# Kernel optimization log

Measured on AMD Instinct MI355X. Metric: run time of the kernel, lower is better.

## Reference

```python
import jax, jax.numpy as jnp
import numpy as np

K2 = 4.0 / 3.0; K4 = 4.10451; K5 = 19.08857; K6 = 254.5553148552
KN = 7.5; WF = 6.0; GA = 3.0; GC = 2.0
BOHR = 0.5291772105638411; HARTREE = 27.211386024367243
C2BOHR = 1.0 / BOHR; C2EV = 0.5 * HARTREE
N_ATOMS = 50000; N_NEIGH = 48; ZMAX = 87; NREF = 7; NFREQ = 23; KCN = 7


def _sp_inv(x):
    # softplus_inverse
    return jnp.float32(np.log(np.expm1(x)))


def setup_inputs() -> dict:
    key = jax.random.key(0)
    ks = jax.random.split(key, 24)
    P = N_ATOMS * N_NEIGH
    u = lambda k, shp, lo, hi: jax.random.uniform(k, shp, jnp.float32, lo, hi)
    Z = jax.random.randint(ks[0], (N_ATOMS,), 0, ZMAX)
    idx_i = jnp.repeat(jnp.arange(N_ATOMS), N_NEIGH)  # center index per pair
    idx_j = jax.random.randint(ks[1], (P,), 0, N_ATOMS)
    r_ij = u(ks[2], (P,), 1.5, 6.0)  # Angstrom
    qa = 0.05 * jax.random.normal(ks[3], (N_ATOMS,), jnp.float32)
    return dict(
        Z=Z, idx_i=idx_i, idx_j=idx_j, r_ij=r_ij, qa=qa,
        s6_raw=_sp_inv(1.0), s8_raw=_sp_inv(1.61679827),
        a1_raw=_sp_inv(0.44959224), a2_raw=_sp_inv(3.35743605),
        scaleq_raw=_sp_inv(1.0),
        refsys=jax.random.randint(ks[4], (ZMAX, NREF), 0, ZMAX),
        zeff=u(ks[5], (ZMAX,), 1.0, 10.0),
        refh=u(ks[6], (ZMAX, NREF), 0.0, 0.3),
        sscale=u(ks[7], (ZMAX,), 0.5, 1.5),
        secaiw=u(ks[8], (ZMAX, NFREQ), 0.0, 1.0),
        gam=u(ks[9], (ZMAX,), 0.05, 0.5),
        ascale=u(ks[10], (ZMAX, NREF), 0.5, 1.5),
        alphaiw=u(ks[11], (ZMAX, NREF, NFREQ), 0.0, 5.0),
        hcount=u(ks[12], (ZMAX, NREF), 0.0, 2.0),
        casimir_polder_weights=u(ks[13], (NFREQ,), 0.0, 0.5),
        rcov=u(ks[14], (ZMAX,), 0.6, 2.5),
        en=u(ks[15], (ZMAX,), 0.5, 4.0),
        ncount_mask=(u(ks[16], (ZMAX, NREF, KCN), 0.0, 1.0) < 0.6).astype(jnp.float32),
        ncount_weight=u(ks[17], (ZMAX, NREF, KCN), 0.5, 2.0),
        cn=u(ks[18], (ZMAX, NREF, KCN), 0.0, 6.0),
        fixgweights=(lambda g: g / jnp.sum(g, -1, keepdims=True))(u(ks[19], (ZMAX, NREF), 0.1, 1.0)),
        refq=u(ks[20], (ZMAX, NREF), -0.2, 0.2),
        sqrt_r4r2=u(ks[21], (ZMAX,), 1.0, 4.0),
    )


def compute_refc6(scaleq, refsys, zeff, refh, sscale, secaiw, gam, ascale, alphaiw, hcount, cpw):
    iz = zeff[refsys]                                   # [Z, nref]
    qref = iz
    qmod = iz + refh * scaleq
    qmod_ = jnp.where(qmod > 1e-8, qmod, 1.0)
    zeta = jnp.where(qmod > 1e-8,
                     jnp.exp(GA * (1.0 - jnp.exp(gam[refsys] * GC * (1.0 - qref / qmod_)))),
                     np.exp(GA).astype(np.float32))
    asec = sscale[refsys][..., None] * secaiw[refsys] * zeta[..., None]  # [Z,nref,nfreq]
    alpha = jnp.maximum(ascale[..., None] * (alphaiw - hcount[..., None] * asec), 0.0)
    return (3.0 / np.pi) * jnp.einsum('iax,jbx,x->ijab', alpha, alpha, cpw)  # [Z,Z,nref,nref]


def reference(Z, idx_i, idx_j, r_ij, qa, s6_raw, s8_raw, a1_raw, a2_raw, scaleq_raw,
              refsys, zeff, refh, sscale, secaiw, gam, ascale, alphaiw, hcount,
              casimir_polder_weights, rcov, en, ncount_mask, ncount_weight, cn,
              fixgweights, refq, sqrt_r4r2):
    n_atoms = qa.shape[0]
    scaleq = jax.nn.softplus(scaleq_raw)
    # refc6 is computed under no_grad in the original module
    refc6 = jax.lax.stop_gradient(compute_refc6(scaleq, refsys, zeff, refh, sscale,
                                                secaiw, gam, ascale, alphaiw, hcount,
                                                casimir_polder_weights))
    r = r_ij * C2BOHR
    Zi = Z[idx_i]; Zj = Z[idx_j]
    # coordination-number contribution per pair, scattered to centers
    rco = K2 * (rcov[Zi] + rcov[Zj])
    den = K4 * jnp.exp(-(jnp.abs(en[Zi] - en[Zj]) + K5) ** 2 / K6)
    tmp = den * 0.5 * (1.0 + jax.lax.erf(-KN * (r - rco) / rco))
    covcn = jax.ops.segment_sum(tmp, idx_i, num_segments=n_atoms)
    # gaussian reference-CN weights [n_atoms, nref]
    gweights = jnp.sum(ncount_mask[Z] * jnp.exp(-WF * ncount_weight[Z] * (covcn[:, None, None] - cn[Z]) ** 2), -1)
    norm = jnp.sum(gweights, -1, keepdims=True)
    gweights = jnp.where(norm > 1e-8, gweights / jnp.where(norm > 1e-8, norm, 1.0), fixgweights[Z])
    # charge scaling zeta [n_atoms, nref]
    iz = zeff[Z][:, None]
    qref = iz + refq[Z] * scaleq
    qmod = iz + qa[:, None]
    qmod_ = jnp.where(qmod > 1e-8, qmod, 1.0)
    zeta = jnp.where(qmod > 1e-8,
                     jnp.exp(GA * (1.0 - jnp.exp(gam[Z][:, None] * GC * (1.0 - qref / qmod_)))),
                     np.exp(GA).astype(np.float32)) * gweights
    zetai = zeta[idx_i]; zetaj = zeta[idx_j]            # [P, nref]
    refc6ij = refc6[Zi, Zj]                             # [P, nref, nref]
    c6ij = jnp.einsum('pab,pa,pb->p', refc6ij, zetai, zetaj)
    r4r2ij = np.float32(np.sqrt(3.0)) * sqrt_r4r2[Zi] * sqrt_r4r2[Zj]
    a1 = jax.nn.softplus(a1_raw); a2 = jax.nn.softplus(a2_raw)
    r0 = a1 * r4r2ij + a2
    oor6 = 1.0 / (r ** 6 + r0 ** 6)
    oor8 = 1.0 / (r ** 8 + r0 ** 8)
    s6 = jax.nn.softplus(s6_raw); s8 = jax.nn.softplus(s8_raw)
    edisp = -c6ij * (s6 * oor6 + s8 * r4r2ij ** 2 * oor8) * C2EV
    eatom = jax.ops.segment_sum(edisp, idx_i, num_segments=n_atoms)
    zeros = jnp.zeros((n_atoms,), r_ij.dtype)  # compute_atomic_quantities=False
    return (eatom, zeros, zeros)
```

## Files before the change

kernel.cpp:

```cpp
#include <hip/hip_runtime.h>
#include <hip/hip_fp16.h>
#include <math.h>

#define NATOMS 50000
#define NNEIGH 48
#define ZMAXV 87
#define NREFV 7
#define NFREQV 23
#define KCNV 7
#define XPAD 24
#define XPADH 32
#define ATOMS_PER_BLOCK 4
#define PAIR_BLOCK (ATOMS_PER_BLOCK * NNEIGH)

#define C2BOHR 1.8897261258369282f
#define C2EV 13.605693012183622f
#define K2C 1.33333333333333333f
#define K4C 4.10451f
#define K5C 19.08857f
#define K6INV (1.0f / 254.5553148552f)
#define KNC 7.5f
#define EXP_GA 20.085536923187668f
#define QRT3 1.3160740129524924f

__device__ __forceinline__ float sp(float x) { return log1pf(expf(x)); }

__global__ __launch_bounds__(256) void k_setup(
    const int* __restrict__ Z, const int* __restrict__ refsys,
    const float* __restrict__ zeff, const float* __restrict__ refh,
    const float* __restrict__ sscale, const float* __restrict__ secaiw,
    const float* __restrict__ gam, const float* __restrict__ ascale,
    const float* __restrict__ alphaiw, const float* __restrict__ hcount,
    const float* __restrict__ rcov, const float* __restrict__ en,
    const float* __restrict__ s6r, const float* __restrict__ s8r,
    const float* __restrict__ a1r, const float* __restrict__ a2r,
    const float* __restrict__ sqr,
    float* __restrict__ scal_out, float* __restrict__ alpha_out,
    float2* __restrict__ re2_out, float* __restrict__ zero_out)
{
    int e = blockIdx.x * 256 + threadIdx.x;
    if (e == 0) {
        scal_out[0] = sp(s6r[0]);
        scal_out[1] = sp(s8r[0]);
        scal_out[2] = sp(a1r[0]);
        scal_out[3] = sp(a2r[0]);
    }
    if (e < 2 * NATOMS) zero_out[e] = 0.0f;
    if (e < NATOMS) {
        int z = Z[e];
        re2_out[e] = make_float2(rcov[z], en[z]);
    }
    if (e < ZMAXV * NREFV * XPAD) {
        int x = e % XPAD;
        int za = e / XPAD;
        float v = 0.0f;
        if (x < NFREQV) {
            float scaleq = sp(sqr[0]);
            int rs = refsys[za];
            float iz = zeff[rs];
            float qmod = iz + refh[za] * scaleq;
            float zeta = (qmod > 1e-8f)
                ? __expf(3.0f * (1.0f - __expf(gam[rs] * 2.0f * (1.0f - iz / qmod))))
                : EXP_GA;
            float asec = sscale[rs] * secaiw[rs * NFREQV + x] * zeta;
            v = fmaxf(ascale[za] * (alphaiw[za * NFREQV + x] - hcount[za] * asec), 0.0f);
        }
        alpha_out[e] = v;
    }
}

__global__ __launch_bounds__(PAIR_BLOCK) void k_atoms(
    const int* __restrict__ Z, const int* __restrict__ idx_j,
    const float* __restrict__ r_ij, const float* __restrict__ qa,
    const float* __restrict__ sqr, const float* __restrict__ zeff,
    const float* __restrict__ gam, const float2* __restrict__ re2,
    const float* __restrict__ nmask, const float* __restrict__ nweight,
    const float* __restrict__ cn, const float* __restrict__ fixg,
    const float* __restrict__ refq, const float* __restrict__ cpw,
    const float* __restrict__ alpha_tab, const float* __restrict__ sr4r2,
    __half* __restrict__ A_out)
{
    __shared__ float sh[PAIR_BLOCK];
    __shared__ float covcn[ATOMS_PER_BLOCK];
    __shared__ float gwl[ATOMS_PER_BLOCK][NREFV];
    __shared__ float ztl[ATOMS_PER_BLOCK][NREFV];
    const int t = threadIdx.x;
    const int a0 = blockIdx.x * ATOMS_PER_BLOCK;

    {
        int p = blockIdx.x * PAIR_BLOCK + t;
        int atom = a0 + (t / NNEIGH);
        float2 rei = re2[atom];
        float2 rej = re2[idx_j[p]];
        float r = r_ij[p] * C2BOHR;
        float rco = K2C * (rei.x + rej.x);
        float d = fabsf(rei.y - rej.y) + K5C;
        float den = K4C * __expf(-d * d * K6INV);
        sh[t] = den * 0.5f * (1.0f + erff(-KNC * (r - rco) / rco));
    }
    __syncthreads();
    if (t < ATOMS_PER_BLOCK) {
        float s = 0.0f;
        for (int k = 0; k < NNEIGH; k++) s += sh[t * NNEIGH + k];
        covcn[t] = s;
    }
    __syncthreads();

    if (t < ATOMS_PER_BLOCK * NREFV) {
        int al = t / NREFV, a = t % NREFV;
        int zl = Z[a0 + al];
        float cc = covcn[al];
        const float* mB = nmask + (zl * NREFV + a) * KCNV;
        const float* wB = nweight + (zl * NREFV + a) * KCNV;
        const float* cB = cn + (zl * NREFV + a) * KCNV;
        float g = 0.0f;
        for (int k = 0; k < KCNV; k++) {
            float dc = cc - cB[k];
            g += mB[k] * __expf(-6.0f * wB[k] * dc * dc);
        }
        gwl[al][a] = g;
    }
    __syncthreads();

    if (t < ATOMS_PER_BLOCK * NREFV) {
        int al = t / NREFV, a = t % NREFV;
        int zl = Z[a0 + al];
        float norm = 0.0f;
        for (int b = 0; b < NREFV; b++) norm += gwl[al][b];
        float w = (norm > 1e-8f) ? (gwl[al][a] / norm) : fixg[zl * NREFV + a];
        float scaleq = sp(sqr[0]);
        float iz = zeff[zl];
        float qref = iz + refq[zl * NREFV + a] * scaleq;
        float qmod = iz + qa[a0 + al];
        float zeta = (qmod > 1e-8f)
            ? __expf(3.0f * (1.0f - __expf(gam[zl] * 2.0f * (1.0f - qref / qmod))))
            : EXP_GA;
        ztl[al][a] = zeta * w;
    }
    __syncthreads();

    if (t < ATOMS_PER_BLOCK * XPADH) {
        int al = t / XPADH, x = t % XPADH;
        int zl = Z[a0 + al];
        float v = 0.0f;
        if (x < NFREQV) {
            float s = 0.0f;
            #pragma unroll
            for (int a = 0; a < NREFV; a++)
                s += ztl[al][a] * alpha_tab[(zl * NREFV + a) * XPAD + x];
            v = s * sqrtf(cpw[x] * 0.9549296585513721f);
        } else if (x == NFREQV) {
            v = QRT3 * sr4r2[zl];
        }
        A_out[(size_t)a0 * XPADH + t] = __float2half(v);
    }
}

__global__ __launch_bounds__(PAIR_BLOCK) void k_pairs(
    const int* __restrict__ idx_j, const float* __restrict__ r_ij,
    const float* __restrict__ scal, const __half* __restrict__ Ah,
    float* __restrict__ eatom)
{
    __shared__ float sh[PAIR_BLOCK];
    __shared__ float Ai[ATOMS_PER_BLOCK][NFREQV];
    __shared__ float Asi[ATOMS_PER_BLOCK];
    const int t = threadIdx.x;
    const int a0 = blockIdx.x * ATOMS_PER_BLOCK;

    if (t < ATOMS_PER_BLOCK * XPADH) {
        int al = t >> 5, x = t & 31;
        float v = __half2float(Ah[(size_t)a0 * XPADH + t]);
        if (x < NFREQV) Ai[al][x] = v;
        else if (x == NFREQV) Asi[al] = v;
    }
    __syncthreads();

    const float s6 = scal[0], s8 = scal[1], a1 = scal[2], a2 = scal[3];

    int p = blockIdx.x * PAIR_BLOCK + t;
    int al = t / NNEIGH;
    int j = idx_j[p];
    float r = r_ij[p] * C2BOHR;

    const float4* Aj4 = (const float4*)(Ah + (size_t)j * XPADH);
    float4 w0 = Aj4[0], w1 = Aj4[1], w2 = Aj4[2];
    float a[24];
    {
        const __half2* h0 = (const __half2*)&w0;
        const __half2* h1 = (const __half2*)&w1;
        const __half2* h2 = (const __half2*)&w2;
        #pragma unroll
        for (int k = 0; k < 4; k++) {
            float2 f0 = __half22float2(h0[k]);
            float2 f1 = __half22float2(h1[k]);
            float2 f2 = __half22float2(h2[k]);
            a[2 * k]      = f0.x; a[2 * k + 1]      = f0.y;
            a[8 + 2 * k]  = f1.x; a[8 + 2 * k + 1]  = f1.y;
            a[16 + 2 * k] = f2.x; a[16 + 2 * k + 1] = f2.y;
        }
    }
    float c6 = 0.0f;
    #pragma unroll
    for (int x = 0; x < NFREQV; x++) c6 += a[x] * Ai[al][x];
    float sj = a[NFREQV];

    float r4r2 = Asi[al] * sj;
    float r0 = a1 * r4r2 + a2;
    float r2 = r * r, r4 = r2 * r2, r6 = r4 * r2, r8 = r4 * r4;
    float p2 = r0 * r0, p4 = p2 * p2, p6 = p4 * p2, p8 = p4 * p4;
    float oor6 = 1.0f / (r6 + p6);
    float oor8 = 1.0f / (r8 + p8);
    float e = -c6 * (s6 * oor6 + s8 * r4r2 * r4r2 * oor8) * C2EV;

    sh[t] = e;
    __syncthreads();
    if (t < ATOMS_PER_BLOCK) {
        float s = 0.0f;
        for (int k = 0; k < NNEIGH; k++) s += sh[t * NNEIGH + k];
        eatom[a0 + t] = s;
    }
}

extern "C" void kernel_launch(void* const* d_in, const int* in_sizes, int n_in,
                              void* d_out, int out_size, void* d_ws, size_t ws_size,
                              hipStream_t stream)
{
    const int*   Z       = (const int*)  d_in[0];
    const int*   idx_j   = (const int*)  d_in[2];
    const float* r_ij    = (const float*)d_in[3];
    const float* qa      = (const float*)d_in[4];
    const float* s6r     = (const float*)d_in[5];
    const float* s8r     = (const float*)d_in[6];
    const float* a1r     = (const float*)d_in[7];
    const float* a2r     = (const float*)d_in[8];
    const float* sqraw   = (const float*)d_in[9];
    const int*   refsys  = (const int*)  d_in[10];
    const float* zeff    = (const float*)d_in[11];
    const float* refh    = (const float*)d_in[12];
    const float* sscale  = (const float*)d_in[13];
    const float* secaiw  = (const float*)d_in[14];
    const float* gam     = (const float*)d_in[15];
    const float* ascale  = (const float*)d_in[16];
    const float* alphaiw = (const float*)d_in[17];
    const float* hcount  = (const float*)d_in[18];
    const float* cpw     = (const float*)d_in[19];
    const float* rcov    = (const float*)d_in[20];
    const float* en      = (const float*)d_in[21];
    const float* nmask   = (const float*)d_in[22];
    const float* nweight = (const float*)d_in[23];
    const float* cn      = (const float*)d_in[24];
    const float* fixg    = (const float*)d_in[25];
    const float* refq    = (const float*)d_in[26];
    const float* sr4r2   = (const float*)d_in[27];

    float* ws    = (float*)d_ws;
    float* scal  = ws;
    float* alpha = ws + 16;
    float2* re2  = (float2*)(ws + 16 + ZMAXV * NREFV * XPAD);
    __half* Ah   = (__half*)(ws + 16 + ZMAXV * NREFV * XPAD + 2 * NATOMS);

    float* eatom = (float*)d_out;
    float* zeros = eatom + NATOMS;

    k_setup<<<391, 256, 0, stream>>>(Z, refsys, zeff, refh, sscale, secaiw, gam,
                                     ascale, alphaiw, hcount, rcov, en,
                                     s6r, s8r, a1r, a2r, sqraw,
                                     scal, alpha, re2, zeros);
    k_atoms<<<NATOMS / ATOMS_PER_BLOCK, PAIR_BLOCK, 0, stream>>>(
        Z, idx_j, r_ij, qa, sqraw, zeff, gam, re2,
        nmask, nweight, cn, fixg, refq, cpw, alpha, sr4r2, Ah);
    k_pairs<<<NATOMS / ATOMS_PER_BLOCK, PAIR_BLOCK, 0, stream>>>(
        idx_j, r_ij, scal, Ah, eatom);
}
```

Before: 177.7 us.

## Process two pairs per thread with eight atoms per block in atom and pair kernels

Each block now covers 8 atoms with 192 threads, and every thread handles two neighbor pairs (p and p+192) in both the coordination-number pass and the C6/energy pass. The atom-descriptor writes switch to half2 stores, and the workspace offsets are realigned with hard-coded byte offsets. The aim is more memory-level parallelism per thread, since each thread has two independent gathers in flight, and fewer blocks. In exchange there is more register pressure and fewer threads overall, and the fixed offsets rely on the workspace layout matching.

After: 180.1 us. Within noise of the previous version (+1.3%).

```diff
diff --git a/kernel.cpp b/kernel.cpp
--- a/kernel.cpp
+++ b/kernel.cpp
@@ -10,8 +10,9 @@
 #define KCNV 7
 #define XPAD 24
 #define XPADH 32
-#define ATOMS_PER_BLOCK 4
-#define PAIR_BLOCK (ATOMS_PER_BLOCK * NNEIGH)
+#define APB 8
+#define TPB 192
+#define PPB (APB * NNEIGH)
 
 #define C2BOHR 1.8897261258369282f
 #define C2EV 13.605693012183622f
@@ -69,7 +70,7 @@
     }
 }
 
-__global__ __launch_bounds__(PAIR_BLOCK) void k_atoms(
+__global__ __launch_bounds__(TPB) void k_atoms(
     const int* __restrict__ Z, const int* __restrict__ idx_j,
     const float* __restrict__ r_ij, const float* __restrict__ qa,
     const float* __restrict__ sqr, const float* __restrict__ zeff,
@@ -78,35 +79,49 @@
     const float* __restrict__ cn, const float* __restrict__ fixg,
     const float* __restrict__ refq, const float* __restrict__ cpw,
     const float* __restrict__ alpha_tab, const float* __restrict__ sr4r2,
-    __half* __restrict__ A_out)
+    __half2* __restrict__ A_out2)
 {
-    __shared__ float sh[PAIR_BLOCK];
-    __shared__ float covcn[ATOMS_PER_BLOCK];
-    __shared__ float gwl[ATOMS_PER_BLOCK][NREFV];
-    __shared__ float ztl[ATOMS_PER_BLOCK][NREFV];
+    __shared__ float sh[PPB];
+    __shared__ float covcn[APB];
+    __shared__ float gwl[APB][NREFV];
+    __shared__ float ztl[APB][NREFV];
     const int t = threadIdx.x;
-    const int a0 = blockIdx.x * ATOMS_PER_BLOCK;
-
-    {
-        int p = blockIdx.x * PAIR_BLOCK + t;
-        int atom = a0 + (t / NNEIGH);
-        float2 rei = re2[atom];
-        float2 rej = re2[idx_j[p]];
-        float r = r_ij[p] * C2BOHR;
-        float rco = K2C * (rei.x + rej.x);
-        float d = fabsf(rei.y - rej.y) + K5C;
-        float den = K4C * __expf(-d * d * K6INV);
-        sh[t] = den * 0.5f * (1.0f + erff(-KNC * (r - rco) / rco));
-    }
-    __syncthreads();
-    if (t < ATOMS_PER_BLOCK) {
+    const int a0 = blockIdx.x * APB;
+
+    {
+        int p0 = blockIdx.x * PPB + t;
+        int p1 = p0 + TPB;
+        int al0 = t / NNEIGH;
+        int j0 = idx_j[p0];
+        int j1 = idx_j[p1];
+        float rr0 = r_ij[p0];
+        float rr1 = r_ij[p1];
+        float2 rej0 = re2[j0];
+        float2 rej1 = re2[j1];
+        float2 rei0 = re2[a0 + al0];
+        float2 rei1 = re2[a0 + al0 + 4];
+
+        float r0 = rr0 * C2BOHR;
+        float rco0 = K2C * (rei0.x + rej0.x);
+        float d0 = fabsf(rei0.y - rej0.y) + K5C;
+        float den0 = K4C * __expf(-d0 * d0 * K6INV);
+        sh[t] = den0 * 0.5f * (1.0f + erff(-KNC * (r0 - rco0) / rco0));
+
+        float r1 = rr1 * C2BOHR;
+        float rco1 = K2C * (rei1.x + rej1.x);
+        float d1 = fabsf(rei1.y - rej1.y) + K5C;
+        float den1 = K4C * __expf(-d1 * d1 * K6INV);
+        sh[t + TPB] = den1 * 0.5f * (1.0f + erff(-KNC * (r1 - rco1) / rco1));
+    }
+    __syncthreads();
+    if (t < APB) {
         float s = 0.0f;
         for (int k = 0; k < NNEIGH; k++) s += sh[t * NNEIGH + k];
         covcn[t] = s;
     }
     __syncthreads();
 
-    if (t < ATOMS_PER_BLOCK * NREFV) {
+    if (t < APB * NREFV) {
         int al = t / NREFV, a = t % NREFV;
         int zl = Z[a0 + al];
         float cc = covcn[al];
@@ -122,7 +137,7 @@
     }
     __syncthreads();
 
-    if (t < ATOMS_PER_BLOCK * NREFV) {
+    if (t < APB * NREFV) {
         int al = t / NREFV, a = t % NREFV;
         int zl = Z[a0 + al];
         float norm = 0.0f;
@@ -139,82 +154,112 @@
     }
     __syncthreads();
 
-    if (t < ATOMS_PER_BLOCK * XPADH) {
-        int al = t / XPADH, x = t % XPADH;
+    if (t < APB * (XPADH / 2)) {
+        int al = t >> 4, xh = t & 15;
+        int x0 = 2 * xh, x1 = 2 * xh + 1;
         int zl = Z[a0 + al];
-        float v = 0.0f;
-        if (x < NFREQV) {
+        float v0 = 0.0f, v1 = 0.0f;
+        if (x0 < NFREQV) {
             float s = 0.0f;
             #pragma unroll
             for (int a = 0; a < NREFV; a++)
-                s += ztl[al][a] * alpha_tab[(zl * NREFV + a) * XPAD + x];
-            v = s * sqrtf(cpw[x] * 0.9549296585513721f);
-        } else if (x == NFREQV) {
-            v = QRT3 * sr4r2[zl];
-        }
-        A_out[(size_t)a0 * XPADH + t] = __float2half(v);
+                s += ztl[al][a] * alpha_tab[(zl * NREFV + a) * XPAD + x0];
+            v0 = s * sqrtf(cpw[x0] * 0.9549296585513721f);
+        }
+        if (x1 < NFREQV) {
+            float s = 0.0f;
+            #pragma unroll
+            for (int a = 0; a < NREFV; a++)
+                s += ztl[al][a] * alpha_tab[(zl * NREFV + a) * XPAD + x1];
+            v1 = s * sqrtf(cpw[x1] * 0.9549296585513721f);
+        } else if (x1 == NFREQV) {
+            v1 = QRT3 * sr4r2[zl];
+        }
+        A_out2[(size_t)(a0 + al) * (XPADH / 2) + xh] = __floats2half2_rn(v0, v1);
     }
 }
 
-__global__ __launch_bounds__(PAIR_BLOCK) void k_pairs(
+__global__ __launch_bounds__(TPB) void k_pairs(
     const int* __restrict__ idx_j, const float* __restrict__ r_ij,
     const float* __restrict__ scal, const __half* __restrict__ Ah,
     float* __restrict__ eatom)
 {
-    __shared__ float sh[PAIR_BLOCK];
-    __shared__ float Ai[ATOMS_PER_BLOCK][NFREQV];
-    __shared__ float Asi[ATOMS_PER_BLOCK];
+    __shared__ float sh[PPB];
+    __shared__ float Ai[APB][NFREQV];
+    __shared__ float Asi[APB];
     const int t = threadIdx.x;
-    const int a0 = blockIdx.x * ATOMS_PER_BLOCK;
-
-    if (t < ATOMS_PER_BLOCK * XPADH) {
-        int al = t >> 5, x = t & 31;
-        float v = __half2float(Ah[(size_t)a0 * XPADH + t]);
+    const int a0 = blockIdx.x * APB;
+
+    {
+        int al = t / XPAD, x = t - al * XPAD;
+        float v = __half2float(Ah[(size_t)(a0 + al) * XPADH + x]);
         if (x < NFREQV) Ai[al][x] = v;
-        else if (x == NFREQV) Asi[al] = v;
+        else Asi[al] = v;
     }
     __syncthreads();
 
     const float s6 = scal[0], s8 = scal[1], a1 = scal[2], a2 = scal[3];
 
-    int p = blockIdx.x * PAIR_BLOCK + t;
-    int al = t / NNEIGH;
-    int j = idx_j[p];
-    float r = r_ij[p] * C2BOHR;
-
-    const float4* Aj4 = (const float4*)(Ah + (size_t)j * XPADH);
-    float4 w0 = Aj4[0], w1 = Aj4[1], w2 = Aj4[2];
-    float a[24];
-    {
-        const __half2* h0 = (const __half2*)&w0;
-        const __half2* h1 = (const __half2*)&w1;
-        const __half2* h2 = (const __half2*)&w2;
+    int p0 = blockIdx.x * PPB + t;
+    int p1 = p0 + TPB;
+    int al0 = t / NNEIGH;
+    int al1 = al0 + 4;
+    int j0 = idx_j[p0];
+    int j1 = idx_j[p1];
+    float rr0 = r_ij[p0];
+    float rr1 = r_ij[p1];
+
+    const float4* P0 = (const float4*)(Ah + (size_t)j0 * XPADH);
+    const float4* P1 = (const float4*)(Ah + (size_t)j1 * XPADH);
+    float4 u0 = P0[0], u1 = P0[1], u2 = P0[2];
+    float4 w0 = P1[0], w1 = P1[1], w2 = P1[2];
+
+    float c60 = 0.0f, c61 = 0.0f, sj0, sj1;
+    {
+        const __half2* hu = (const __half2*)&u0;
+        const __half2* a2p[3] = { (const __half2*)&u0, (const __half2*)&u1, (const __half2*)&u2 };
+        const __half2* b2p[3] = { (const __half2*)&w0, (const __half2*)&w1, (const __half2*)&w2 };
+        (void)hu;
         #pragma unroll
-        for (int k = 0; k < 4; k++) {
-            float2 f0 = __half22float2(h0[k]);
-            float2 f1 = __half22float2(h1[k]);
-            float2 f2 = __half22float2(h2[k]);
-            a[2 * k]      = f0.x; a[2 * k + 1]      = f0.y;
-            a[8 + 2 * k]  = f1.x; a[8 + 2 * k + 1]  = f1.y;
-            a[16 + 2 * k] = f2.x; a[16 + 2 * k + 1] = f2.y;
-        }
-    }
-    float c6 = 0.0f;
-    #pragma unroll
-    for (int x = 0; x < NFREQV; x++) c6 += a[x] * Ai[al][x];
-    float sj = a[NFREQV];
-
-    float r4r2 = Asi[al] * sj;
-    float r0 = a1 * r4r2 + a2;
-    float r2 = r * r, r4 = r2 * r2, r6 = r4 * r2, r8 = r4 * r4;
-    float p2 = r0 * r0, p4 = p2 * p2, p6 = p4 * p2, p8 = p4 * p4;
-    float oor6 = 1.0f / (r6 + p6);
-    float oor8 = 1.0f / (r8 + p8);
-    float e = -c6 * (s6 * oor6 + s8 * r4r2 * r4r2 * oor8) * C2EV;
-
-    sh[t] = e;
-    __syncthreads();
-    if (t < ATOMS_PER_BLOCK) {
+        for (int seg = 0; seg < 3; seg++) {
+            #pragma unroll
+            for (int k = 0; k < 4; k++) {
+                int x = seg * 8 + 2 * k;
+                float2 fa = __half22float2(a2p[seg][k]);
+                float2 fb = __half22float2(b2p[seg][k]);
+                if (x < NFREQV)      c60 += fa.x * Ai[al0][x];
+                else                 sj0 = fa.x;
+                if (x + 1 < NFREQV)  c60 += fa.y * Ai[al0][x + 1];
+                else if (x + 1 == NFREQV) sj0 = fa.y;
+                if (x < NFREQV)      c61 += fb.x * Ai[al1][x];
+                if (x + 1 < NFREQV)  c61 += fb.y * Ai[al1][x + 1];
+                else if (x + 1 == NFREQV) sj1 = fb.y;
+            }
+        }
+    }
+
+    float e0, e1;
+    {
+        float r = rr0 * C2BOHR;
+        float r4r2 = Asi[al0] * sj0;
+        float r0v = a1 * r4r2 + a2;
+        float r2 = r * r, r4 = r2 * r2, r6 = r4 * r2, r8 = r4 * r4;
+        float p2 = r0v * r0v, p4 = p2 * p2, p6 = p4 * p2, p8 = p4 * p4;
+        e0 = -c60 * (s6 / (r6 + p6) + s8 * r4r2 * r4r2 / (r8 + p8)) * C2EV;
+    }
+    {
+        float r = rr1 * C2BOHR;
+        float r4r2 = Asi[al1] * sj1;
+        float r0v = a1 * r4r2 + a2;
+        float r2 = r * r, r4 = r2 * r2, r6 = r4 * r2, r8 = r4 * r4;
+        float p2 = r0v * r0v, p4 = p2 * p2, p6 = p4 * p2, p8 = p4 * p4;
+        e1 = -c61 * (s6 / (r6 + p6) + s8 * r4r2 * r4r2 / (r8 + p8)) * C2EV;
+    }
+
+    sh[t] = e0;
+    sh[t + TPB] = e1;
+    __syncthreads();
+    if (t < APB) {
         float s = 0.0f;
         for (int k = 0; k < NNEIGH; k++) s += sh[t * NNEIGH + k];
         eatom[a0 + t] = s;
@@ -253,11 +298,11 @@
     const float* refq    = (const float*)d_in[26];
     const float* sr4r2   = (const float*)d_in[27];
 
-    float* ws    = (float*)d_ws;
-    float* scal  = ws;
-    float* alpha = ws + 16;
-    float2* re2  = (float2*)(ws + 16 + ZMAXV * NREFV * XPAD);
-    __half* Ah   = (__half*)(ws + 16 + ZMAXV * NREFV * XPAD + 2 * NATOMS);
+    char* wsb = (char*)d_ws;
+    float*  scal  = (float*)(wsb);
+    float*  alpha = (float*)(wsb + 64);
+    float2* re2   = (float2*)(wsb + 58528);
+    __half* Ah    = (__half*)(wsb + 458752);
 
     float* eatom = (float*)d_out;
     float* zeros = eatom + NATOMS;
@@ -266,9 +311,9 @@
                                      ascale, alphaiw, hcount, rcov, en,
                                      s6r, s8r, a1r, a2r, sqraw,
                                      scal, alpha, re2, zeros);
-    k_atoms<<<NATOMS / ATOMS_PER_BLOCK, PAIR_BLOCK, 0, stream>>>(
+    k_atoms<<<NATOMS / APB, TPB, 0, stream>>>(
         Z, idx_j, r_ij, qa, sqraw, zeff, gam, re2,
-        nmask, nweight, cn, fixg, refq, cpw, alpha, sr4r2, Ah);
-    k_pairs<<<NATOMS / ATOMS_PER_BLOCK, PAIR_BLOCK, 0, stream>>>(
+        nmask, nweight, cn, fixg, refq, cpw, alpha, sr4r2, (__half2*)Ah);
+    k_pairs<<<NATOMS / APB, TPB, 0, stream>>>(
         idx_j, r_ij, scal, Ah, eatom);
 }
```
